# Kernel optimization log

Hardware: AMD Instinct MI355X
Metric: run time of the kernel (lower is better)

## Reference

```python
import jax, jax.numpy as jnp
import numpy as np


def _cost_volume(x, y, maxdisp):
    # x, y: [N, C, H, W] left/right feature maps.
    # Replicates the torch loop:
    #   for i in range(D): d = D-1-i
    #     cost[:, :C, d, :, i:W]  = x[:, :, :, i:W]
    #     cost[:, C:, d, :, i:]   = y_pad[:, :, :, :W+D-i]   (y zero-padded to W+D)
    # =>  cost_x[d, j] = x[..., j]      if D-1-d <= j < W   else 0
    #     cost_y[d, j] = y[..., j-(D-1-d)] if 0 <= j-(D-1-d) < W else 0
    N, C, H, W = x.shape
    D = maxdisp
    Wc = W + D
    d = jnp.arange(D)
    i = (D - 1) - d                      # shift per depth plane, [D]
    j = jnp.arange(Wc)                   # output width coords, [Wc]

    # left-image half: same columns, masked per depth plane
    xp = jnp.pad(x, ((0, 0), (0, 0), (0, 0), (0, D)))          # [N,C,H,Wc]
    mask_x = (j[None, :] >= i[:, None]) & (j[None, :] < W)      # [D,Wc]
    cost_x = xp[:, :, None, :, :] * mask_x[None, None, :, None, :].astype(x.dtype)

    # right-image half: shifted gather with zero fill
    jy = j[None, :] - i[:, None]                                # [D,Wc]
    valid = (jy >= 0) & (jy < W)
    idx = jnp.clip(jy, 0, W - 1)
    y_g = y[:, :, :, idx]                                       # [N,C,H,D,Wc]
    cost_y = jnp.where(valid[None, None, None, :, :], y_g, jnp.zeros((), x.dtype))
    cost_y = cost_y.transpose(0, 1, 3, 2, 4)                    # [N,C,D,H,Wc]

    return jnp.concatenate([cost_x, cost_y], axis=1)            # [N,2C,D,H,Wc]


def setup_inputs() -> dict:
    key = jax.random.key(0)
    k1, k2 = jax.random.split(key)
    N, C, H, W = 2, 32, 64, 128
    x = jax.random.normal(k1, (N, C, H, W), dtype=jnp.float32)
    y = jax.random.normal(k2, (N, C, H, W), dtype=jnp.float32)
    return {"x": x, "y": y, "maxdisp": 48}


def reference(x, y, maxdisp):
    return _cost_volume(x, y, maxdisp)
```

## Files before the change

kernel.cpp:

```cpp
#include <hip/hip_runtime.h>

constexpr int N  = 2;
constexpr int C  = 32;
constexpr int H  = 64;
constexpr int W  = 128;
constexpr int D  = 48;
constexpr int Wc = W + D;
constexpr int Wc4 = Wc / 4;
constexpr int C2 = 2 * C;
constexpr long long TOTAL4 = (long long)N * C2 * D * H * Wc4;

__global__ __launch_bounds__(256)
void cost_volume_kernel(const float* __restrict__ x,
                        const float* __restrict__ y,
                        float* __restrict__ out)
{
    long long tid = (long long)blockIdx.x * blockDim.x + threadIdx.x;
    if (tid >= TOTAL4) return;

    int v  = (int)(tid % Wc4);
    long long r = tid / Wc4;
    int j0 = v * 4;

    int h  = (int)(r % H);
    long long t = r / H;
    int d  = (int)(t % D);
    long long t2 = t / D;
    int cc = (int)(t2 % C2);
    int n  = (int)(t2 / C2);

    int i = D - 1 - d;

    float4 o;
    float* po = (float*)&o;

    if (cc < C) {
        const float* __restrict__ xrow = x + (((long long)(n * C + cc) * H + h) * W);
        #pragma unroll
        for (int k = 0; k < 4; ++k) {
            int j = j0 + k;
            int jc = j < W ? j : (W - 1);
            float val = xrow[jc];
            po[k] = (j >= i && j < W) ? val : 0.0f;
        }
    } else {
        const float* __restrict__ yrow = y + (((long long)(n * C + (cc - C)) * H + h) * W);
        #pragma unroll
        for (int k = 0; k < 4; ++k) {
            int jy = j0 + k - i;
            int jyc = jy < 0 ? 0 : (jy >= W ? W - 1 : jy);
            float val = yrow[jyc];
            po[k] = (jy >= 0 && jy < W) ? val : 0.0f;
        }
    }

    reinterpret_cast<float4*>(out)[tid] = o;
}

extern "C" void kernel_launch(void* const* d_in, const int* in_sizes, int n_in,
                              void* d_out, int out_size, void* d_ws, size_t ws_size,
                              hipStream_t stream)
{
    const float* x = (const float*)d_in[0];
    const float* y = (const float*)d_in[1];
    float* out = (float*)d_out;

    int blocks = (int)((TOTAL4 + 255) / 256);
    cost_volume_kernel<<<dim3(blocks), dim3(256), 0, stream>>>(x, y, out);
}
```

Baseline: 321.8 us.

## Stage each input row in LDS and emit all depth planes per block

Each block now loads one (n, channel, h) input row into shared memory with zero padding, then writes that row's entries for all D depth planes. The padding lets the shifted y half be read without branches. This removes the per-element 64-bit index division and repeated global gathers and reuses each input row across 48 planes. In exchange, the float4 vectorized stores become scalar stores, each block's writes are strided across planes, and the grid shrinks to 8192 blocks.

```diff
diff --git a/kernel.cpp b/kernel.cpp
--- a/kernel.cpp
+++ b/kernel.cpp
@@ -1,60 +1,70 @@
 #include <hip/hip_runtime.h>
 
-constexpr int N  = 2;
-constexpr int C  = 32;
-constexpr int H  = 64;
-constexpr int W  = 128;
-constexpr int D  = 48;
-constexpr int Wc = W + D;
-constexpr int Wc4 = Wc / 4;
-constexpr int C2 = 2 * C;
-constexpr long long TOTAL4 = (long long)N * C2 * D * H * Wc4;
+constexpr int N   = 2;
+constexpr int C   = 32;
+constexpr int H   = 64;
+constexpr int W   = 128;
+constexpr int D   = 48;
+constexpr int Wc  = W + D;
+constexpr int C2  = 2 * C;
+constexpr int PLANE = D * Wc;
+constexpr int NBLOCKS = N * C2 * H;
 
 __global__ __launch_bounds__(256)
 void cost_volume_kernel(const float* __restrict__ x,
                         const float* __restrict__ y,
                         float* __restrict__ out)
 {
-    long long tid = (long long)blockIdx.x * blockDim.x + threadIdx.x;
-    if (tid >= TOTAL4) return;
+    __shared__ float row[224];
 
-    int v  = (int)(tid % Wc4);
-    long long r = tid / Wc4;
-    int j0 = v * 4;
+    unsigned b   = blockIdx.x;
+    unsigned tid = threadIdx.x;
 
-    int h  = (int)(r % H);
-    long long t = r / H;
-    int d  = (int)(t % D);
-    long long t2 = t / D;
-    int cc = (int)(t2 % C2);
-    int n  = (int)(t2 / C2);
+    unsigned h  = b % H;
+    unsigned t  = b / H;
+    unsigned cc = t % C2;
+    unsigned n  = t / C2;
 
-    int i = D - 1 - d;
+    bool is_x = cc < C;
 
-    float4 o;
-    float* po = (float*)&o;
+    if (is_x) {
+        if (tid < 128)
+            row[tid] = x[((n * C + cc) * H + h) * W + tid];
+        else if (tid < 224)
+            row[tid] = 0.0f;
+    } else {
+        if (tid < 48)
+            row[tid] = 0.0f;
+        else if (tid < 176)
+            row[tid] = y[((n * C + (cc - C)) * H + h) * W + (tid - 48)];
+        else if (tid < 224)
+            row[tid] = 0.0f;
+    }
+    __syncthreads();
 
-    if (cc < C) {
-        const float* __restrict__ xrow = x + (((long long)(n * C + cc) * H + h) * W);
-        #pragma unroll
-        for (int k = 0; k < 4; ++k) {
-            int j = j0 + k;
-            int jc = j < W ? j : (W - 1);
-            float val = xrow[jc];
-            po[k] = (j >= i && j < W) ? val : 0.0f;
+    unsigned base = (n * C2 + cc) * (unsigned)(D * H * Wc) + h * (unsigned)Wc;
+    float* __restrict__ outp = out + base;
+
+    if (is_x) {
+        #pragma unroll 4
+        for (unsigned p = tid; p < (unsigned)PLANE; p += 256) {
+            unsigned d = p / (unsigned)Wc;
+            unsigned j = p - d * (unsigned)Wc;
+            unsigned i = (unsigned)(D - 1) - d;
+            float v = row[j];
+            v = (j >= i) ? v : 0.0f;
+            outp[d * (unsigned)(H * Wc) + j] = v;
         }
     } else {
-        const float* __restrict__ yrow = y + (((long long)(n * C + (cc - C)) * H + h) * W);
-        #pragma unroll
-        for (int k = 0; k < 4; ++k) {
-            int jy = j0 + k - i;
-            int jyc = jy < 0 ? 0 : (jy >= W ? W - 1 : jy);
-            float val = yrow[jyc];
-            po[k] = (jy >= 0 && jy < W) ? val : 0.0f;
+        #pragma unroll 4
+        for (unsigned p = tid; p < (unsigned)PLANE; p += 256) {
+            unsigned d = p / (unsigned)Wc;
+            unsigned j = p - d * (unsigned)Wc;
+            unsigned i = (unsigned)(D - 1) - d;
+            float v = row[48 + j - i];
+            outp[d * (unsigned)(H * Wc) + j] = v;
         }
     }
-
-    reinterpret_cast<float4*>(out)[tid] = o;
 }
 
 extern "C" void kernel_launch(void* const* d_in, const int* in_sizes, int n_in,
@@ -65,6 +75,5 @@
     const float* y = (const float*)d_in[1];
     float* out = (float*)d_out;
 
-    int blocks = (int)((TOTAL4 + 255) / 256);
-    cost_volume_kernel<<<dim3(blocks), dim3(256), 0, stream>>>(x, y, out);
+    cost_volume_kernel<<<dim3(NBLOCKS), dim3(256), 0, stream>>>(x, y, out);
 }
```

Measured after the change: 303.8 us. 1.06x faster.

## Assign one block per (n,c,d) plane with vectorized loads and nontemporal stores

Applied to the files above, without the earlier changes.

The kernel now launches one 256-thread block per (n, channel, depth) output plane. Each thread loops over 11 float4 chunks of the H×Wc plane, which replaces the 64-bit div/mod index decomposition with cheap per-block constants. The x half reads a single float4 per chunk instead of four scalar loads, and every output store uses a nontemporal hint to keep the large write-only volume from polluting the cache. The work per thread is fixed at 11×256 = 2816 = H*Wc/4, so the indexing is hardcoded to these shapes.

```diff
diff --git a/kernel.cpp b/kernel.cpp
--- a/kernel.cpp
+++ b/kernel.cpp
@@ -1,60 +1,79 @@
 #include <hip/hip_runtime.h>
 
-constexpr int N  = 2;
-constexpr int C  = 32;
-constexpr int H  = 64;
-constexpr int W  = 128;
-constexpr int D  = 48;
-constexpr int Wc = W + D;
-constexpr int Wc4 = Wc / 4;
-constexpr int C2 = 2 * C;
-constexpr long long TOTAL4 = (long long)N * C2 * D * H * Wc4;
+constexpr int N    = 2;
+constexpr int C    = 32;
+constexpr int H    = 64;
+constexpr int W    = 128;
+constexpr int D    = 48;
+constexpr int Wc   = W + D;
+constexpr int C2   = 2 * C;
+constexpr int HWc  = H * Wc;
+constexpr int VEC  = HWc / 4;
+constexpr int W4   = W / 4;
+constexpr int NBLOCKS = N * C2 * D;
+
+typedef float vf4 __attribute__((ext_vector_type(4)));
 
 __global__ __launch_bounds__(256)
 void cost_volume_kernel(const float* __restrict__ x,
                         const float* __restrict__ y,
                         float* __restrict__ out)
 {
-    long long tid = (long long)blockIdx.x * blockDim.x + threadIdx.x;
-    if (tid >= TOTAL4) return;
+    unsigned b   = blockIdx.x;
+    unsigned tid = threadIdx.x;
 
-    int v  = (int)(tid % Wc4);
-    long long r = tid / Wc4;
-    int j0 = v * 4;
-
-    int h  = (int)(r % H);
-    long long t = r / H;
-    int d  = (int)(t % D);
-    long long t2 = t / D;
-    int cc = (int)(t2 % C2);
-    int n  = (int)(t2 / C2);
-
+    unsigned d  = b % D;
+    unsigned t  = b / D;
+    unsigned cc = t % C2;
+    unsigned n  = t / C2;
     int i = D - 1 - d;
 
-    float4 o;
-    float* po = (float*)&o;
+    vf4* __restrict__ outv = reinterpret_cast<vf4*>(out) + (size_t)b * VEC;
 
-    if (cc < C) {
-        const float* __restrict__ xrow = x + (((long long)(n * C + cc) * H + h) * W);
+    bool is_x = cc < C;
+
+    if (is_x) {
+        const float* __restrict__ xp = x + ((size_t)(n * C + cc) * H) * W;
         #pragma unroll
-        for (int k = 0; k < 4; ++k) {
-            int j = j0 + k;
-            int jc = j < W ? j : (W - 1);
-            float val = xrow[jc];
-            po[k] = (j >= i && j < W) ? val : 0.0f;
+        for (int it = 0; it < 11; ++it) {
+            unsigned q = tid + 256u * it;
+            unsigned h = q / 44u;
+            unsigned v = q - 44u * h;
+            int j0 = 4 * (int)v;
+
+            unsigned vc = v < (unsigned)W4 ? v : 0u;
+            vf4 ld = *reinterpret_cast<const vf4*>(xp + h * W + 4u * vc);
+
+            bool inw = v < (unsigned)W4;
+            vf4 o;
+            o.x = (inw && j0 + 0 >= i) ? ld.x : 0.0f;
+            o.y = (inw && j0 + 1 >= i) ? ld.y : 0.0f;
+            o.z = (inw && j0 + 2 >= i) ? ld.z : 0.0f;
+            o.w = (inw && j0 + 3 >= i) ? ld.w : 0.0f;
+            __builtin_nontemporal_store(o, &outv[q]);
         }
     } else {
-        const float* __restrict__ yrow = y + (((long long)(n * C + (cc - C)) * H + h) * W);
+        const float* __restrict__ yp = y + ((size_t)(n * C + (cc - C)) * H) * W;
         #pragma unroll
-        for (int k = 0; k < 4; ++k) {
-            int jy = j0 + k - i;
-            int jyc = jy < 0 ? 0 : (jy >= W ? W - 1 : jy);
-            float val = yrow[jyc];
-            po[k] = (jy >= 0 && jy < W) ? val : 0.0f;
+        for (int it = 0; it < 11; ++it) {
+            unsigned q = tid + 256u * it;
+            unsigned h = q / 44u;
+            unsigned v = q - 44u * h;
+            int j0 = 4 * (int)v;
+            int jy0 = j0 - i;
+
+            const float* __restrict__ yrow = yp + h * W;
+            vf4 o;
+            #pragma unroll
+            for (int k = 0; k < 4; ++k) {
+                int jy  = jy0 + k;
+                int jyc = jy < 0 ? 0 : (jy >= W ? W - 1 : jy);
+                float val = yrow[jyc];
+                o[k] = (jy >= 0 && jy < W) ? val : 0.0f;
+            }
+            __builtin_nontemporal_store(o, &outv[q]);
         }
     }
-
-    reinterpret_cast<float4*>(out)[tid] = o;
 }
 
 extern "C" void kernel_launch(void* const* d_in, const int* in_sizes, int n_in,
@@ -65,6 +84,5 @@
     const float* y = (const float*)d_in[1];
     float* out = (float*)d_out;
 
-    int blocks = (int)((TOTAL4 + 255) / 256);
-    cost_volume_kernel<<<dim3(blocks), dim3(256), 0, stream>>>(x, y, out);
+    cost_volume_kernel<<<dim3(NBLOCKS), dim3(256), 0, stream>>>(x, y, out);
 }
```

Measured after the change: 311.6 us. -3.2%, faster.
